# Optimization experiments

Hardware: AMD Instinct MI355X
Metric: run time of the kernel (lower is better)

The kernel has to match this reference:

```python
import jax, jax.numpy as jnp
import numpy as np
from jax.scipy.special import gammaln

WARMUP = 365
KERNEL = 15
PRECISION = 1e-5

# [lo, hi] per parameter, order: BETA FC K0 K1 K2 LP PERC UZL TT CFMAX CFR CWH A THETA
PARAM_RANGES = np.array([
    [1.0, 6.0], [50.0, 1000.0], [0.05, 0.9], [0.01, 0.5], [0.001, 0.2],
    [0.2, 1.0], [0.0, 10.0], [0.0, 100.0], [-2.5, 2.5], [0.5, 10.0],
    [0.0, 0.1], [0.0, 0.2], [0.0, 2.9], [0.0, 6.5],
], dtype=np.float32)


def scale_params(parameters):
    lo = jnp.asarray(PARAM_RANGES[:, 0])
    hi = jnp.asarray(PARAM_RANGES[:, 1])
    return lo + parameters * (hi - lo)  # [n_grid, 14]


def run_hbv(p_all, pet_all, t_all, phys, init_state):
    beta, fc, k0, k1, k2 = phys[:, 0], phys[:, 1], phys[:, 2], phys[:, 3], phys[:, 4]
    lp, pperc, uzl, tt = phys[:, 5], phys[:, 6], phys[:, 7], phys[:, 8]
    cfmax, cfr, cwh = phys[:, 9], phys[:, 10], phys[:, 11]

    def step(state, inp):
        snowpack, meltwater, sm, suz, slz = state
        precip, potent, tempre = inp
        is_rain = (tempre >= tt).astype(jnp.float32)
        rain = precip * is_rain
        snow = precip * (1.0 - is_rain)
        snowpack = snowpack + snow
        melt = jnp.minimum(jnp.maximum(cfmax * (tempre - tt), 0.0), snowpack)
        meltwater = meltwater + melt
        snowpack = snowpack - melt
        refreezing = jnp.minimum(jnp.maximum(cfr * cfmax * (tt - tempre), 0.0), meltwater)
        snowpack = snowpack + refreezing
        meltwater = meltwater - refreezing
        to_soil = jnp.maximum(meltwater - cwh * snowpack, 0.0)
        meltwater = meltwater - to_soil
        soil_wetness = jnp.clip((sm / fc) ** beta, 0.0, 1.0)
        recharge = (rain + to_soil) * soil_wetness
        sm = sm + rain + to_soil - recharge
        excess = jnp.maximum(sm - fc, 0.0)
        sm = sm - excess
        evap_factor = jnp.clip(sm / (lp * fc), 0.0, 1.0)
        et_act = jnp.minimum(sm, potent * evap_factor)
        sm = jnp.maximum(sm - et_act, PRECISION)
        suz = suz + recharge + excess
        perc = jnp.minimum(suz, pperc)
        suz = suz - perc
        q0 = k0 * jnp.maximum(suz - uzl, 0.0)
        suz = suz - q0
        q1 = k1 * suz
        suz = suz - q1
        slz = slz + perc
        q2 = k2 * slz
        slz = slz - q2
        return (snowpack, meltwater, sm, suz, slz), q0 + q1 + q2

    final_state, q_sim = jax.lax.scan(step, init_state, (p_all, pet_all, t_all))
    return q_sim, final_state


def uh_gamma(a, b, len_uh):
    # a, b: [n_grid]; returns normalized gamma-pdf unit hydrograph [len_uh, n_grid]
    aa = jax.nn.relu(a) + 0.1
    theta = jax.nn.relu(b) + 0.5
    t = jnp.arange(0.5, len_uh, dtype=jnp.float32)[:, None]  # [K, 1]
    log_w = (aa - 1.0) * jnp.log(t) - t / theta - gammaln(aa) - aa * jnp.log(theta)
    w = jnp.exp(log_w)
    return w / w.sum(axis=0, keepdims=True)


def hbv_forward(x, parameters):
    n_grid = x.shape[1]
    phys = scale_params(parameters)
    init = tuple(jnp.full((n_grid,), 0.001, dtype=jnp.float32) for _ in range(5))
    # warmup under no_grad -> stop_gradient on resulting states
    xw = x[:WARMUP]
    _, warm_state = run_hbv(xw[..., 0], xw[..., 1], xw[..., 2], phys, init)
    warm_state = jax.lax.stop_gradient(warm_state)
    xm = x[WARMUP:]
    q_sim, _ = run_hbv(xm[..., 0], xm[..., 1], xm[..., 2], phys, warm_state)  # [n_step, n_grid]
    # gamma unit-hydrograph routing (causal conv over time, per grid cell)
    uh = uh_gamma(phys[:, 12], phys[:, 13], KERNEL)  # [K, n_grid]
    n_step = q_sim.shape[0]
    qp = jnp.pad(q_sim, ((KERNEL - 1, 0), (0, 0)))
    qs = jnp.zeros_like(q_sim)
    for k in range(KERNEL):
        qs = qs + uh[k] * jax.lax.dynamic_slice_in_dim(qp, KERNEL - 1 - k, n_step, 0)
    return qs[..., None]  # [n_step, n_grid, 1]


def setup_inputs() -> dict:
    key = jax.random.key(0)
    k1, k2, k3, k4 = jax.random.split(key, 4)
    T, G = 2190, 10000  # 365 warmup + 1825 simulated days, 10k basins
    precip = jax.random.uniform(k1, (T, G), dtype=jnp.float32) * 10.0  # mm/day
    pet = jax.random.uniform(k2, (T, G), dtype=jnp.float32) * 5.0      # mm/day
    temp = jax.random.normal(k3, (T, G), dtype=jnp.float32) * 10.0     # deg C
    x = jnp.stack([precip, pet, temp], axis=-1)
    parameters = jax.random.uniform(k4, (G, 14), dtype=jnp.float32)
    return {"x": x, "parameters": parameters}


def reference(x, parameters):
    return hbv_forward(x, parameters)
```

## Files before the change

### kernel.cpp

```cpp
#include <hip/hip_runtime.h>

#define WARMUP  365
#define NSTEP   1825
#define TTOT    2190
#define KERNEL_ 15
#define CH      15
#define NCH     3
#define SLOTF   256
#define NCHUNK  146

#define WAIT_RING() asm volatile("s_waitcnt vmcnt(30)" ::: "memory")

typedef __attribute__((address_space(1))) const void g_void;
typedef __attribute__((address_space(3))) void l_void;

__global__ __launch_bounds__(64) void hbv_fused_kernel(
    const float* __restrict__ x,
    const float* __restrict__ params,
    float* __restrict__ out,
    int G)
{
    __shared__ float lds[NCH * CH * SLOTF];

    const int lane = threadIdx.x;
    const int g0   = blockIdx.x * 64;
    const int g    = g0 + lane;
    if (g >= G) return;

    const float* pr = params + (size_t)g * 14;
    const float beta  = 1.0f   + pr[0]  * 5.0f;
    const float fc    = 50.0f  + pr[1]  * 950.0f;
    const float k0    = 0.05f  + pr[2]  * 0.85f;
    const float k1    = 0.01f  + pr[3]  * 0.49f;
    const float k2    = 0.001f + pr[4]  * 0.199f;
    const float lp    = 0.2f   + pr[5]  * 0.8f;
    const float pperc =          pr[6]  * 10.0f;
    const float uzl   =          pr[7]  * 100.0f;
    const float tt    = -2.5f  + pr[8]  * 5.0f;
    const float cfmax = 0.5f   + pr[9]  * 9.5f;
    const float cfr   =          pr[10] * 0.1f;
    const float cwh   =          pr[11] * 0.2f;
    const float ra    =          pr[12] * 2.9f;
    const float rb    =          pr[13] * 6.5f;

    const float aa = fmaxf(ra, 0.0f) + 0.1f;
    const float th = fmaxf(rb, 0.0f) + 0.5f;
    const float inv_th = 1.0f / th;
    float w[KERNEL_];
    float ws = 0.0f;
    #pragma unroll
    for (int k = 0; k < KERNEL_; k++) {
        const float tk = 0.5f + (float)k;
        const float lw = (aa - 1.0f) * __logf(tk) - tk * inv_th;
        w[k] = __expf(lw);
        ws += w[k];
    }
    const float inv_ws = 1.0f / ws;
    #pragma unroll
    for (int k = 0; k < KERNEL_; k++) w[k] *= inv_ws;

    const float inv_fc   = 1.0f / fc;
    const float inv_lpfc = 1.0f / (lp * fc);
    const float cfrx     = cfr * cfmax;

    float sp  = 0.001f;
    float mw  = 0.001f;
    float sm  = 0.001f;
    float suz = 0.001f;
    float slz = 0.001f;

    auto step = [&](float precip, float pet, float temp) -> float {
        const float dt   = temp - tt;
        const float rain = (dt >= 0.0f) ? precip : 0.0f;
        sp += precip - rain;
        const float melt = fminf(fmaxf(cfmax * dt, 0.0f), sp);
        mw += melt;
        sp -= melt;
        const float refr = fminf(fmaxf(-cfrx * dt, 0.0f), mw);
        sp += refr;
        mw -= refr;
        const float tosoil = fmaxf(mw - cwh * sp, 0.0f);
        mw -= tosoil;
        const float r   = sm * inv_fc;
        const float wet = fminf(__expf(beta * __logf(r)), 1.0f);
        const float inflow = rain + tosoil;
        const float rech   = inflow * wet;
        sm += inflow - rech;
        const float exc = fmaxf(sm - fc, 0.0f);
        sm -= exc;
        const float ef = fminf(sm * inv_lpfc, 1.0f);
        const float et = fminf(sm, pet * ef);
        sm = fmaxf(sm - et, 1e-5f);
        suz += rech + exc;
        const float perc = fminf(suz, pperc);
        suz -= perc;
        const float q0 = k0 * fmaxf(suz - uzl, 0.0f);
        suz -= q0;
        const float q1 = k1 * suz;
        suz -= q1;
        slz += perc;
        const float q2 = k2 * slz;
        slz -= q2;
        return q0 + q1 + q2;
    };

    const unsigned rowb   = (unsigned)G * 12u;
    const unsigned maxoff = (unsigned)TTOT * rowb - 16u;
    const unsigned roff   = (unsigned)g0 * 12u + (unsigned)lane * 16u;
    const char* xb = (const char*)x;

    auto refill = [&](int slot, unsigned off0) {
        unsigned off = off0;
        #pragma unroll
        for (int j = 0; j < CH; ++j) {
            const unsigned o = off > maxoff ? maxoff : off;
            __builtin_amdgcn_global_load_lds(
                (g_void*)(xb + o),
                (l_void*)&lds[(slot * CH + j) * SLOTF],
                16, 0, 0);
            off += rowb;
        }
    };
    auto fetch3 = [&](int slot, int j, float& p, float& e, float& t) {
        const float* s = &lds[(slot * CH + j) * SLOTF + lane * 3];
        p = s[0]; e = s[1]; t = s[2];
    };

    float buf[KERNEL_];
    #pragma unroll
    for (int k = 0; k < KERNEL_; k++) buf[k] = 0.0f;

    unsigned offnext = roff;
    refill(0, offnext); offnext += (unsigned)CH * rowb;
    refill(1, offnext); offnext += (unsigned)CH * rowb;
    refill(2, offnext); offnext += (unsigned)CH * rowb;

    int slot = 0;

    for (int c = 0; c < 24; ++c) {
        WAIT_RING();
        #pragma unroll
        for (int j = 0; j < CH; ++j) {
            float p, e, t; fetch3(slot, j, p, e, t);
            (void)step(p, e, t);
        }
        refill(slot, offnext); offnext += (unsigned)CH * rowb;
        slot = (slot == NCH - 1) ? 0 : slot + 1;
    }

    {
        WAIT_RING();
        #pragma unroll
        for (int j = 0; j < 5; ++j) {
            float p, e, t; fetch3(slot, j, p, e, t);
            (void)step(p, e, t);
        }
        #pragma unroll
        for (int j = 0; j < 10; ++j) {
            float p, e, t; fetch3(slot, 5 + j, p, e, t);
            const float q = step(p, e, t);
            buf[j] = q;
            float acc = 0.0f;
            #pragma unroll
            for (int k = 0; k < KERNEL_; ++k)
                acc = fmaf(w[k], buf[(j - k + KERNEL_) % KERNEL_], acc);
            out[(size_t)j * G + g] = acc;
        }
        refill(slot, offnext); offnext += (unsigned)CH * rowb;
        slot = (slot == NCH - 1) ? 0 : slot + 1;
    }

    int m0 = 10;
    for (int c = 25; c < NCHUNK; ++c) {
        WAIT_RING();
        #pragma unroll
        for (int j = 0; j < CH; ++j) {
            float p, e, t; fetch3(slot, j, p, e, t);
            const float q = step(p, e, t);
            const int pos = (10 + j) % KERNEL_;
            buf[pos] = q;
            float acc = 0.0f;
            #pragma unroll
            for (int k = 0; k < KERNEL_; ++k)
                acc = fmaf(w[k], buf[(pos - k + KERNEL_) % KERNEL_], acc);
            out[(size_t)(m0 + j) * G + g] = acc;
        }
        refill(slot, offnext); offnext += (unsigned)CH * rowb;
        slot = (slot == NCH - 1) ? 0 : slot + 1;
        m0 += CH;
    }
}

extern "C" void kernel_launch(void* const* d_in, const int* in_sizes, int n_in,
                              void* d_out, int out_size, void* d_ws, size_t ws_size,
                              hipStream_t stream) {
    const float* x      = (const float*)d_in[0];
    const float* params = (const float*)d_in[1];
    float* out = (float*)d_out;
    const int G = in_sizes[1] / 14;
    const int blocks = (G + 63) / 64;
    hbv_fused_kernel<<<blocks, 64, 0, stream>>>(x, params, out, G);
}
```

Measured before the change: 610.8 us.

## Split producer/consumer waves: one wave runs recurrence, other loads, precomputes snow terms, convolves

The kernel moves to two waves per block. Wave 0 runs only the serial HBV state recurrence, reading precomputed rain, snow, melt-rate and PET values from LDS and writing runoff into an LDS ring. Wave 1 issues the global-to-LDS prefetch, precomputes the snow-partition terms, and does the 15-tap unit-hydrograph convolution and the output stores. The aim is to take memory waits, convolution and store work off the latency-bound recurrence chain. In exchange it adds a block barrier every chunk, leaves the prefetch only two chunks ahead, and costs extra LDS.

```diff
diff --git a/kernel.cpp b/kernel.cpp
--- a/kernel.cpp
+++ b/kernel.cpp
@@ -5,24 +5,25 @@
 #define TTOT    2190
 #define KERNEL_ 15
 #define CH      15
-#define NCH     3
-#define SLOTF   256
+#define ROWF    256
 #define NCHUNK  146
-
-#define WAIT_RING() asm volatile("s_waitcnt vmcnt(30)" ::: "memory")
 
 typedef __attribute__((address_space(1))) const void g_void;
 typedef __attribute__((address_space(3))) void l_void;
 
-__global__ __launch_bounds__(64) void hbv_fused_kernel(
+__global__ __launch_bounds__(128) void hbv_fused_kernel(
     const float* __restrict__ x,
     const float* __restrict__ params,
     float* __restrict__ out,
     int G)
 {
-    __shared__ float lds[NCH * CH * SLOTF];
-
-    const int lane = threadIdx.x;
+    __shared__ __align__(16) float  raw  [3 * CH * ROWF];
+    __shared__ __align__(16) float4 pre4 [2 * CH * 64];
+    __shared__ __align__(16) float  qring[2 * CH * 64];
+
+    const int tid  = threadIdx.x;
+    const int wv   = tid >> 6;
+    const int lane = tid & 63;
     const int g0   = blockIdx.x * 64;
     const int g    = g0 + lane;
     if (g >= G) return;
@@ -43,6 +44,10 @@
     const float ra    =          pr[12] * 2.9f;
     const float rb    =          pr[13] * 6.5f;
 
+    const float inv_fc   = 1.0f / fc;
+    const float inv_lpfc = 1.0f / (lp * fc);
+    const float cfrx     = cfr * cfmax;
+
     const float aa = fmaxf(ra, 0.0f) + 0.1f;
     const float th = fmaxf(rb, 0.0f) + 0.5f;
     const float inv_th = 1.0f / th;
@@ -51,143 +56,136 @@
     #pragma unroll
     for (int k = 0; k < KERNEL_; k++) {
         const float tk = 0.5f + (float)k;
-        const float lw = (aa - 1.0f) * __logf(tk) - tk * inv_th;
-        w[k] = __expf(lw);
+        w[k] = __expf((aa - 1.0f) * __logf(tk) - tk * inv_th);
         ws += w[k];
     }
     const float inv_ws = 1.0f / ws;
     #pragma unroll
     for (int k = 0; k < KERNEL_; k++) w[k] *= inv_ws;
 
-    const float inv_fc   = 1.0f / fc;
-    const float inv_lpfc = 1.0f / (lp * fc);
-    const float cfrx     = cfr * cfmax;
-
-    float sp  = 0.001f;
-    float mw  = 0.001f;
-    float sm  = 0.001f;
-    float suz = 0.001f;
-    float slz = 0.001f;
-
-    auto step = [&](float precip, float pet, float temp) -> float {
-        const float dt   = temp - tt;
-        const float rain = (dt >= 0.0f) ? precip : 0.0f;
-        sp += precip - rain;
-        const float melt = fminf(fmaxf(cfmax * dt, 0.0f), sp);
-        mw += melt;
-        sp -= melt;
-        const float refr = fminf(fmaxf(-cfrx * dt, 0.0f), mw);
-        sp += refr;
-        mw -= refr;
-        const float tosoil = fmaxf(mw - cwh * sp, 0.0f);
-        mw -= tosoil;
-        const float r   = sm * inv_fc;
-        const float wet = fminf(__expf(beta * __logf(r)), 1.0f);
-        const float inflow = rain + tosoil;
-        const float rech   = inflow * wet;
-        sm += inflow - rech;
-        const float exc = fmaxf(sm - fc, 0.0f);
-        sm -= exc;
-        const float ef = fminf(sm * inv_lpfc, 1.0f);
-        const float et = fminf(sm, pet * ef);
-        sm = fmaxf(sm - et, 1e-5f);
-        suz += rech + exc;
-        const float perc = fminf(suz, pperc);
-        suz -= perc;
-        const float q0 = k0 * fmaxf(suz - uzl, 0.0f);
-        suz -= q0;
-        const float q1 = k1 * suz;
-        suz -= q1;
-        slz += perc;
-        const float q2 = k2 * slz;
-        slz -= q2;
-        return q0 + q1 + q2;
-    };
+    float sp = 0.001f, mw = 0.001f, sm = 0.001f, suz = 0.001f, slz = 0.001f;
+
+    float cbuf[KERNEL_];
+    #pragma unroll
+    for (int k = 0; k < KERNEL_; k++) cbuf[k] = 0.0f;
 
     const unsigned rowb   = (unsigned)G * 12u;
     const unsigned maxoff = (unsigned)TTOT * rowb - 16u;
     const unsigned roff   = (unsigned)g0 * 12u + (unsigned)lane * 16u;
     const char* xb = (const char*)x;
 
-    auto refill = [&](int slot, unsigned off0) {
-        unsigned off = off0;
+    auto refill = [&](int s, int h) {
+        const unsigned hb = (unsigned)(h * CH) * rowb + roff;
         #pragma unroll
         for (int j = 0; j < CH; ++j) {
-            const unsigned o = off > maxoff ? maxoff : off;
+            unsigned off = hb + (unsigned)j * rowb;
+            off = off > maxoff ? maxoff : off;
             __builtin_amdgcn_global_load_lds(
-                (g_void*)(xb + o),
-                (l_void*)&lds[(slot * CH + j) * SLOTF],
+                (g_void*)(xb + off),
+                (l_void*)&raw[(s * CH + j) * ROWF],
                 16, 0, 0);
-            off += rowb;
         }
     };
-    auto fetch3 = [&](int slot, int j, float& p, float& e, float& t) {
-        const float* s = &lds[(slot * CH + j) * SLOTF + lane * 3];
-        p = s[0]; e = s[1]; t = s[2];
-    };
-
-    float buf[KERNEL_];
-    #pragma unroll
-    for (int k = 0; k < KERNEL_; k++) buf[k] = 0.0f;
-
-    unsigned offnext = roff;
-    refill(0, offnext); offnext += (unsigned)CH * rowb;
-    refill(1, offnext); offnext += (unsigned)CH * rowb;
-    refill(2, offnext); offnext += (unsigned)CH * rowb;
-
-    int slot = 0;
-
-    for (int c = 0; c < 24; ++c) {
-        WAIT_RING();
+
+    auto precompute = [&](int s, int b) {
+        const float* rowbase = &raw[s * CH * ROWF];
+        float4* dst = &pre4[b * (CH * 64) + lane];
         #pragma unroll
         for (int j = 0; j < CH; ++j) {
-            float p, e, t; fetch3(slot, j, p, e, t);
-            (void)step(p, e, t);
+            const float* row = rowbase + j * ROWF + lane * 3;
+            const float p = row[0];
+            const float e = row[1];
+            const float t = row[2];
+            const float dt   = t - tt;
+            const float rain = (dt >= 0.0f) ? p : 0.0f;
+            float4 o;
+            o.x = rain;
+            o.y = p - rain;
+            o.z = fmaxf(cfmax * dt, 0.0f) - fmaxf(-cfrx * dt, 0.0f);
+            o.w = e;
+            dst[j * 64] = o;
         }
-        refill(slot, offnext); offnext += (unsigned)CH * rowb;
-        slot = (slot == NCH - 1) ? 0 : slot + 1;
-    }
-
-    {
-        WAIT_RING();
-        #pragma unroll
-        for (int j = 0; j < 5; ++j) {
-            float p, e, t; fetch3(slot, j, p, e, t);
-            (void)step(p, e, t);
+    };
+
+    if (wv == 1) { refill(0, 0); refill(1, 1); }
+    __syncthreads();
+    if (wv == 1) precompute(0, 0);
+
+    float* outp = out + g;
+
+    for (int c = 0; c <= NCHUNK; ++c) {
+        __syncthreads();
+
+        if (wv == 0) {
+            if (c < NCHUNK) {
+                const float4* pv = &pre4[(c & 1) * (CH * 64) + lane];
+                float* qw = &qring[(c & 1) * (CH * 64) + lane];
+                #pragma unroll
+                for (int j = 0; j < CH; ++j) {
+                    const float4 v = pv[j * 64];
+                    const float rain = v.x, snow = v.y, mr = v.z, pet = v.w;
+                    sp += snow;
+                    const float melt = fminf(fmaxf(mr, 0.0f), sp);
+                    mw += melt; sp -= melt;
+                    const float refr = fminf(fmaxf(-mr, 0.0f), mw);
+                    sp += refr; mw -= refr;
+                    const float tosoil = fmaxf(mw - cwh * sp, 0.0f);
+                    mw -= tosoil;
+                    const float r   = sm * inv_fc;
+                    const float wet = fminf(__expf(beta * __logf(r)), 1.0f);
+                    const float inflow = rain + tosoil;
+                    const float rech   = inflow * wet;
+                    sm += inflow - rech;
+                    const float exc = fmaxf(sm - fc, 0.0f);
+                    sm -= exc;
+                    const float ef = fminf(sm * inv_lpfc, 1.0f);
+                    const float et = fminf(sm, pet * ef);
+                    sm = fmaxf(sm - et, 1e-5f);
+                    suz += rech + exc;
+                    const float perc = fminf(suz, pperc);
+                    suz -= perc;
+                    const float q0 = k0 * fmaxf(suz - uzl, 0.0f);
+                    suz -= q0;
+                    const float q1 = k1 * suz;
+                    suz -= q1;
+                    slz += perc;
+                    const float q2 = k2 * slz;
+                    slz -= q2;
+                    qw[j * 64] = q0 + q1 + q2;
+                }
+            }
+        } else {
+            if (c + 2 < NCHUNK) refill((c + 2) % 3, c + 2);
+            if (c + 1 < NCHUNK) precompute((c + 1) % 3, (c + 1) & 1);
+            const int h = c - 1;
+            if (h >= 24) {
+                const float* qs = &qring[(h & 1) * (CH * 64) + lane];
+                if (h == 24) {
+                    #pragma unroll
+                    for (int j = 5; j < CH; ++j) {
+                        const int m = j - 5;
+                        cbuf[m] = qs[j * 64];
+                        float acc = 0.0f;
+                        #pragma unroll
+                        for (int k = 0; k < KERNEL_; ++k)
+                            acc = fmaf(w[k], cbuf[((m - k) % 15 + 15) % 15], acc);
+                        out[(size_t)m * G + g] = acc;
+                    }
+                    outp = out + (size_t)10 * G + g;
+                } else {
+                    #pragma unroll
+                    for (int j = 0; j < CH; ++j) {
+                        cbuf[(j + 10) % 15] = qs[j * 64];
+                        float acc = 0.0f;
+                        #pragma unroll
+                        for (int k = 0; k < KERNEL_; ++k)
+                            acc = fmaf(w[k], cbuf[((j + 10 - k) % 15 + 15) % 15], acc);
+                        outp[(size_t)j * G] = acc;
+                    }
+                    outp += (size_t)CH * G;
+                }
+            }
         }
-        #pragma unroll
-        for (int j = 0; j < 10; ++j) {
-            float p, e, t; fetch3(slot, 5 + j, p, e, t);
-            const float q = step(p, e, t);
-            buf[j] = q;
-            float acc = 0.0f;
-            #pragma unroll
-            for (int k = 0; k < KERNEL_; ++k)
-                acc = fmaf(w[k], buf[(j - k + KERNEL_) % KERNEL_], acc);
-            out[(size_t)j * G + g] = acc;
-        }
-        refill(slot, offnext); offnext += (unsigned)CH * rowb;
-        slot = (slot == NCH - 1) ? 0 : slot + 1;
-    }
-
-    int m0 = 10;
-    for (int c = 25; c < NCHUNK; ++c) {
-        WAIT_RING();
-        #pragma unroll
-        for (int j = 0; j < CH; ++j) {
-            float p, e, t; fetch3(slot, j, p, e, t);
-            const float q = step(p, e, t);
-            const int pos = (10 + j) % KERNEL_;
-            buf[pos] = q;
-            float acc = 0.0f;
-            #pragma unroll
-            for (int k = 0; k < KERNEL_; ++k)
-                acc = fmaf(w[k], buf[(pos - k + KERNEL_) % KERNEL_], acc);
-            out[(size_t)(m0 + j) * G + g] = acc;
-        }
-        refill(slot, offnext); offnext += (unsigned)CH * rowb;
-        slot = (slot == NCH - 1) ? 0 : slot + 1;
-        m0 += CH;
     }
 }
 
@@ -199,5 +197,5 @@
     float* out = (float*)d_out;
     const int G = in_sizes[1] / 14;
     const int blocks = (G + 63) / 64;
-    hbv_fused_kernel<<<blocks, 64, 0, stream>>>(x, params, out, G);
+    hbv_fused_kernel<<<blocks, 128, 0, stream>>>(x, params, out, G);
 }
```

Measured after the change: 590.7 us. 1.03x faster.
